# Performance work log

Measured on AMD Instinct MI355X. Metric: run time of the kernel, lower is better.

The kernel has to match this reference:

```python
import jax, jax.numpy as jnp
import numpy as np

TANH_CLIP = 10.0
TEMP = 1.0


def setup_inputs() -> dict:
    key = jax.random.key(0)
    ks = jax.random.split(key, 8)
    B, N, E, H, SC = 1024, 1000, 128, 8, 256
    dk = E // H
    context = jax.random.normal(ks[0], (B, 1, E), dtype=jnp.float32)
    step_context = jax.random.normal(ks[1], (B, 1, SC), dtype=jnp.float32)
    # scale weights so tanh/softmax stay in a sane numeric range
    W_step = jax.random.normal(ks[2], (E, SC), dtype=jnp.float32) * 0.05
    glimpse_K = jax.random.normal(ks[3], (H, B, 1, N, dk), dtype=jnp.float32)
    glimpse_V = jax.random.normal(ks[4], (H, B, 1, N, dk), dtype=jnp.float32)
    logit_K = jax.random.normal(ks[5], (B, 1, N, E), dtype=jnp.float32)
    W_out = jax.random.normal(ks[6], (E, E), dtype=jnp.float32) * 0.05
    mask = jax.random.randint(ks[7], (B, 1, N), 0, 2).astype(bool)
    mask = mask.at[:, :, 0].set(False)  # guarantee at least one feasible node
    return {"context": context, "step_context": step_context, "W_step": W_step,
            "glimpse_K": glimpse_K, "glimpse_V": glimpse_V, "logit_K": logit_K,
            "W_out": W_out, "mask": mask}


def reference(context, step_context, W_step, glimpse_K, glimpse_V, logit_K, W_out, mask):
    B, S, E = context.shape          # S = num_steps = 1
    H = glimpse_K.shape[0]
    dk = E // H
    neg_inf = jnp.float32(-jnp.inf)
    # query = context_node_projected + project_step_context(step_context)
    query = context + jnp.einsum('bsc,ec->bse', step_context, W_step)  # [B,S,E]
    # split heads: glimpse_Q -> [H,B,S,dk] (the singleton q-dim of the torch code is folded)
    Q = query.reshape(B, S, H, dk).transpose(2, 0, 1, 3)
    # compatibility [H,B,S,N]
    compat = jnp.einsum('hbsk,hbsnk->hbsn', Q, glimpse_K) / jnp.sqrt(jnp.float32(dk))
    compat = jnp.where(mask[None], neg_inf, compat)       # mask_inner
    attn = jax.nn.softmax(compat, axis=-1)
    heads = jnp.einsum('hbsn,hbsnk->hbsk', attn, glimpse_V)  # [H,B,S,dk]
    glimpse = heads.transpose(1, 2, 0, 3).reshape(B, S, E)   # concat heads
    glimpse = jnp.einsum('bse,oe->bso', glimpse, W_out)      # project_out
    # logits against logit_K  [B,S,N]
    logits = jnp.einsum('bse,bsne->bsn', glimpse, logit_K) / jnp.sqrt(jnp.float32(E))
    logits = jnp.tanh(logits) * jnp.float32(TANH_CLIP)       # tanh clipping
    logits = jnp.where(mask, neg_inf, logits)                # mask_logits
    log_p = jax.nn.log_softmax(logits / jnp.float32(TEMP), axis=-1)
    return log_p
```

## Files before the change

### kernel.cpp

```cpp
#include <hip/hip_runtime.h>
#include <hip/hip_bf16.h>
#include <math.h>

#define NB  1024
#define NN  1000
#define NE  128
#define NH  8
#define NDK 16
#define NSC 256

typedef __attribute__((ext_vector_type(4))) float f32x4;

__device__ __forceinline__ f32x4 ld4(const float* p) {
    return *reinterpret_cast<const f32x4*>(p);
}

__global__ __launch_bounds__(128)
void query_kernel(const float* __restrict__ ctx, const float* __restrict__ stepc,
                  const float* __restrict__ Wstep, float* __restrict__ q_ws)
{
    const int b = blockIdx.x, t = threadIdx.x;
    __shared__ float sc[NSC];
    sc[t] = stepc[b * NSC + t];
    sc[t + 128] = stepc[b * NSC + t + 128];
    __syncthreads();
    float acc = ctx[b * NE + t];
    const float4* w4 = reinterpret_cast<const float4*>(Wstep + (size_t)t * NSC);
    #pragma unroll 8
    for (int c4 = 0; c4 < NSC / 4; ++c4) {
        float4 w = w4[c4];
        acc += sc[4*c4] * w.x + sc[4*c4+1] * w.y + sc[4*c4+2] * w.z + sc[4*c4+3] * w.w;
    }
    q_ws[b * NE + t] = acc;
}

__global__ __launch_bounds__(256)
void attn_kernel(const float* __restrict__ q_ws,
                 const float* __restrict__ gK, const float* __restrict__ gV,
                 const unsigned char* __restrict__ mask,
                 float* __restrict__ heads_ws)
{
    const int bid = blockIdx.x;
    const int h = bid & (NH - 1);
    const int b = bid >> 3;
    const int t = threadIdx.x;
    const int w = t >> 6, lane = t & 63;
    const int qq  = lane & 3;
    const int rsl = lane >> 2;

    __shared__ float wmax[4], wsum[4];
    __shared__ __align__(16) float wred[4][16];

    const unsigned int* mw = reinterpret_cast<const unsigned int*>(mask);
    const bool m_i32 = (__ballot(mw[lane] <= 1u) == ~0ull);
    const int* mask_i = reinterpret_cast<const int*>(mask);

    const f32x4 qv = ld4(q_ws + (size_t)b * NE + h * NDK + qq * 4);

    int msk[16];
    #pragma unroll
    for (int i = 0; i < 16; ++i) {
        const int n = w * 16 + i * 64 + rsl;
        const bool dead = (n >= NN);
        const int nn = dead ? 0 : n;
        int mk = m_i32 ? (mask_i[(size_t)b * NN + nn] != 0)
                       : (mask[(size_t)b * NN + nn] != 0);
        msk[i] = mk | (dead ? 1 : 0);
    }

    const float* Kb = gK + (size_t)(h * NB + b) * NN * NDK;
    float pp[16];
    #pragma unroll
    for (int i = 0; i < 16; ++i) {
        const int n = w * 16 + i * 64 + rsl;
        const int nn = msk[i] ? 0 : n;
        f32x4 kv = ld4(Kb + (size_t)nn * NDK + qq * 4);
        pp[i] = kv.x*qv.x + kv.y*qv.y + kv.z*qv.z + kv.w*qv.w;
    }
    float sc[16];
    #pragma unroll
    for (int i = 0; i < 16; ++i) {
        float p = pp[i];
        p += __shfl_xor(p, 1);
        p += __shfl_xor(p, 2);
        sc[i] = msk[i] ? -INFINITY : p * 0.25f;
    }

    float m = sc[0];
    #pragma unroll
    for (int i = 1; i < 16; ++i) m = fmaxf(m, sc[i]);
    #pragma unroll
    for (int off = 32; off > 0; off >>= 1) m = fmaxf(m, __shfl_xor(m, off));
    if (lane == 0) wmax[w] = m;
    __syncthreads();
    const float M = fmaxf(fmaxf(wmax[0], wmax[1]), fmaxf(wmax[2], wmax[3]));

    float e[16], ls = 0.f;
    #pragma unroll
    for (int i = 0; i < 16; ++i) { e[i] = expf(sc[i] - M); ls += e[i]; }
    #pragma unroll
    for (int off = 32; off > 0; off >>= 1) ls += __shfl_xor(ls, off);
    if (lane == 0) wsum[w] = ls;

    const float* Vb = gV + (size_t)(h * NB + b) * NN * NDK;
    f32x4 acc = {0.f, 0.f, 0.f, 0.f};
    #pragma unroll
    for (int i = 0; i < 16; ++i) {
        const int n = w * 16 + i * 64 + rsl;
        const float p = e[i];
        const int nn = (p == 0.f) ? 0 : n;
        f32x4 vv = ld4(Vb + (size_t)nn * NDK + qq * 4);
        acc.x += p * vv.x; acc.y += p * vv.y; acc.z += p * vv.z; acc.w += p * vv.w;
    }
    #pragma unroll
    for (int off = 4; off < 64; off <<= 1) {
        acc.x += __shfl_xor(acc.x, off);
        acc.y += __shfl_xor(acc.y, off);
        acc.z += __shfl_xor(acc.z, off);
        acc.w += __shfl_xor(acc.w, off);
    }
    if (lane < 4) *reinterpret_cast<f32x4*>(&wred[w][lane * 4]) = acc;
    __syncthreads();

    if (t < NDK) {
        const float S = (wsum[0] + wsum[1] + wsum[2] + wsum[3]) * 0.25f;
        const float r = wred[0][t] + wred[1][t] + wred[2][t] + wred[3][t];
        heads_ws[(size_t)b * NE + h * NDK + t] = r / S;
    }
}

__global__ __launch_bounds__(512)
void logits_kernel(const float* __restrict__ heads_ws, const float* __restrict__ Wout,
                   const float* __restrict__ lK, const unsigned char* __restrict__ mask,
                   __hip_bfloat16* __restrict__ out)
{
    const int b = blockIdx.x, t = threadIdx.x;
    const int w = t >> 6, lane = t & 63;
    __shared__ __align__(16) float g[NE];
    __shared__ __align__(16) float gout[NE];
    __shared__ float red[8];
    __shared__ float Mv, LSv;

    const unsigned int* mw = reinterpret_cast<const unsigned int*>(mask);
    const bool m_i32 = (__ballot(mw[lane] <= 1u) == ~0ull);
    const int* mask_i = reinterpret_cast<const int*>(mask);

    if (t < NE) g[t] = heads_ws[(size_t)b * NE + t];
    __syncthreads();

    if (t < NE) {
        float acc = 0.f;
        const float4* w4 = reinterpret_cast<const float4*>(Wout + (size_t)t * NE);
        const float4* g4 = reinterpret_cast<const float4*>(g);
        #pragma unroll 8
        for (int e4 = 0; e4 < NE / 4; ++e4) {
            float4 wv = w4[e4]; float4 gg = g4[e4];
            acc += wv.x*gg.x + wv.y*gg.y + wv.z*gg.z + wv.w*gg.w;
        }
        gout[t] = acc;
    }
    __syncthreads();

    const f32x4* go4 = reinterpret_cast<const f32x4*>(gout);
    float lv[2];
    #pragma unroll
    for (int i = 0; i < 2; ++i) {
        const int n = t + 512 * i;
        const bool live = (n < NN);
        const int nidx = live ? n : 0;
        int mkd = m_i32 ? (mask_i[(size_t)b * NN + nidx] != 0)
                        : (mask[(size_t)b * NN + nidx] != 0);
        mkd |= (live ? 0 : 1);
        const int nn = mkd ? 0 : n;
        const float* lp = lK + ((size_t)b * NN + nn) * NE;
        float acc = 0.f;
        #pragma unroll
        for (int c4 = 0; c4 < NE / 4; ++c4) {
            f32x4 x = ld4(lp + 4 * c4);
            f32x4 gv = go4[c4];
            acc += x.x*gv.x + x.y*gv.y + x.z*gv.z + x.w*gv.w;
        }
        float val = tanhf(acc * 0.08838834764831845f) * 10.0f;
        lv[i] = mkd ? -3.0e38f : val;
    }

    float m = fmaxf(lv[0], lv[1]);
    #pragma unroll
    for (int off = 32; off > 0; off >>= 1) m = fmaxf(m, __shfl_xor(m, off));
    if (lane == 0) red[w] = m;
    __syncthreads();
    if (t == 0) {
        float mm = red[0];
        #pragma unroll
        for (int i = 1; i < 8; ++i) mm = fmaxf(mm, red[i]);
        Mv = mm;
    }
    __syncthreads();
    const float M = Mv;
    float s = expf(lv[0] - M) + expf(lv[1] - M);
    #pragma unroll
    for (int off = 32; off > 0; off >>= 1) s += __shfl_xor(s, off);
    if (lane == 0) red[w] = s;
    __syncthreads();
    if (t == 0) {
        float ss = 0.f;
        #pragma unroll
        for (int i = 0; i < 8; ++i) ss += red[i];
        LSv = M + logf(ss);
    }
    __syncthreads();
    const float LS = LSv;
    #pragma unroll
    for (int i = 0; i < 2; ++i) {
        const int n = t + 512 * i;
        if (n < NN)
            out[(size_t)b * NN + n] = __float2bfloat16(lv[i] - LS);
    }
}

__global__ __launch_bounds__(256, 4)
void evrp_decoder_fused(const float* __restrict__ ctx, const float* __restrict__ stepc,
                        const float* __restrict__ Wstep, const float* __restrict__ gK,
                        const float* __restrict__ gV, const float* __restrict__ lK,
                        const float* __restrict__ Wout, const unsigned char* __restrict__ mask,
                        __hip_bfloat16* __restrict__ out)
{
    const int b = blockIdx.x;
    const int t = threadIdx.x;
    __shared__ __align__(16) float q[NE];
    __shared__ __align__(16) float sc_l[NH * NN];
    __shared__ __align__(16) float g[NE];
    __shared__ __align__(16) float gout[NE];
    __shared__ __align__(16) float red[256];
    __shared__ __align__(16) float ovl[1024];
    __shared__ float mh[NH];
    __shared__ float rinv[NH];
    __shared__ float Mv, Sv;
    __shared__ int mtype;

    if (t == 0) {
        const unsigned int* mi = reinterpret_cast<const unsigned int*>(mask);
        int ok = 1;
        for (int i = 0; i < 64; ++i) ok = ok && (mi[i] <= 1u);
        mtype = ok;
    }
    red[t] = stepc[b * NSC + t];
    __syncthreads();
    const int m_i32 = mtype;
    if (t < NE) {
        float acc = ctx[b * NE + t];
        const float4* w4 = reinterpret_cast<const float4*>(Wstep + t * NSC);
        #pragma unroll 8
        for (int c4 = 0; c4 < NSC / 4; ++c4) {
            float4 w = w4[c4];
            acc += red[c4*4+0]*w.x + red[c4*4+1]*w.y + red[c4*4+2]*w.z + red[c4*4+3]*w.w;
        }
        q[t] = acc;
    }
    __syncthreads();
    const int* mask_i = reinterpret_cast<const int*>(mask);
    for (int n = t; n < NN; n += 256) {
        bool mk = m_i32 ? (mask_i[b * NN + n] != 0) : (mask[b * NN + n] != 0);
        if (mk) {
            #pragma unroll
            for (int h = 0; h < NH; ++h) sc_l[h * NN + n] = -INFINITY;
        } else {
            #pragma unroll
            for (int h = 0; h < NH; ++h) {
                const float4* k4 = reinterpret_cast<const float4*>(gK + (((size_t)h*NB + b)*NN + n)*NDK);
                const float4* q4 = reinterpret_cast<const float4*>(q + h * NDK);
                float acc = 0.f;
                #pragma unroll
                for (int i = 0; i < 4; ++i) {
                    float4 kv = k4[i]; float4 qv = q4[i];
                    acc += kv.x*qv.x + kv.y*qv.y + kv.z*qv.z + kv.w*qv.w;
                }
                sc_l[h * NN + n] = acc * 0.25f;
            }
        }
    }
    __syncthreads();
    {
        const int h = t >> 5, i = t & 31;
        float m = -INFINITY;
        for (int n = i; n < NN; n += 32) m = fmaxf(m, sc_l[h * NN + n]);
        red[t] = m;
        __syncthreads();
        if (t < NH) {
            float mm = -INFINITY;
            for (int i2 = 0; i2 < 32; ++i2) mm = fmaxf(mm, red[t * 32 + i2]);
            mh[t] = mm;
        }
        __syncthreads();
        const float mhh = mh[h];
        float s = 0.f;
        for (int n = i; n < NN; n += 32) {
            float ev = expf(sc_l[h * NN + n] - mhh);
            sc_l[h * NN + n] = ev;
            s += ev;
        }
        red[t] = s;
        __syncthreads();
        if (t < NH) {
            float ss = 0.f;
            for (int i2 = 0; i2 < 32; ++i2) ss += red[t * 32 + i2];
            rinv[t] = 1.0f / ss;
        }
        __syncthreads();
    }
    {
        float4* hp4 = reinterpret_cast<float4*>(ovl);
        const int h = t >> 5, rem = t & 31, kq = rem >> 3, j = rem & 7;
        const float* vbase = gV + (((size_t)h * NB + b) * NN) * NDK + kq * 4;
        float4 acc = {0.f, 0.f, 0.f, 0.f};
        for (int n = j; n < NN; n += 8) {
            float p = sc_l[h * NN + n];
            if (p != 0.f) {
                float4 v = *reinterpret_cast<const float4*>(vbase + (size_t)n * NDK);
                acc.x += p*v.x; acc.y += p*v.y; acc.z += p*v.z; acc.w += p*v.w;
            }
        }
        hp4[(h * 4 + kq) * 8 + j] = acc;
    }
    __syncthreads();
    if (t < NE) {
        const int h = t >> 4, k = t & 15, kq = k >> 2, kc = k & 3;
        float s = 0.f;
        #pragma unroll
        for (int j = 0; j < 8; ++j) s += ovl[((h * 4 + kq) * 8 + j) * 4 + kc];
        g[t] = s * rinv[h];
    }
    __syncthreads();
    if (t < NE) {
        float acc = 0.f;
        const float4* w4 = reinterpret_cast<const float4*>(Wout + t * NE);
        const float4* g4 = reinterpret_cast<const float4*>(g);
        #pragma unroll 8
        for (int e4 = 0; e4 < NE / 4; ++e4) {
            float4 w = w4[e4]; float4 gg = g4[e4];
            acc += w.x*gg.x + w.y*gg.y + w.z*gg.z + w.w*gg.w;
        }
        gout[t] = acc;
    }
    __syncthreads();
    float* llds = ovl;
    for (int n = t; n < NN; n += 256) {
        bool mk = m_i32 ? (mask_i[b * NN + n] != 0) : (mask[b * NN + n] != 0);
        float val;
        if (mk) val = -INFINITY;
        else {
            const float4* lk4 = reinterpret_cast<const float4*>(lK + ((size_t)b * NN + n) * NE);
            const float4* go4 = reinterpret_cast<const float4*>(gout);
            float acc = 0.f;
            #pragma unroll 8
            for (int e4 = 0; e4 < NE / 4; ++e4) {
                float4 lvv = lk4[e4]; float4 gv = go4[e4];
                acc += lvv.x*gv.x + lvv.y*gv.y + lvv.z*gv.z + lvv.w*gv.w;
            }
            val = tanhf(acc * 0.08838834764831845f) * 10.0f;
        }
        llds[n] = val;
    }
    __syncthreads();
    {
        float m = -INFINITY;
        for (int n = t; n < NN; n += 256) m = fmaxf(m, llds[n]);
        red[t] = m;
        __syncthreads();
        for (int s2 = 128; s2 > 0; s2 >>= 1) {
            if (t < s2) red[t] = fmaxf(red[t], red[t + s2]);
            __syncthreads();
        }
        if (t == 0) Mv = red[0];
        __syncthreads();
        const float M = Mv;
        float s = 0.f;
        for (int n = t; n < NN; n += 256) s += expf(llds[n] - M);
        red[t] = s;
        __syncthreads();
        for (int s2 = 128; s2 > 0; s2 >>= 1) {
            if (t < s2) red[t] += red[t + s2];
            __syncthreads();
        }
        if (t == 0) Sv = logf(red[0]);
        __syncthreads();
        const float LS = M + Sv;
        for (int n = t; n < NN; n += 256) {
            float l = llds[n];
            float r = (l == -INFINITY) ? -3.0e38f : (l - LS);
            out[(size_t)b * NN + n] = __float2bfloat16(r);
        }
    }
}

extern "C" void kernel_launch(void* const* d_in, const int* in_sizes, int n_in,
                              void* d_out, int out_size, void* d_ws, size_t ws_size,
                              hipStream_t stream) {
    const float* ctx   = (const float*)d_in[0];
    const float* stepc = (const float*)d_in[1];
    const float* Wstep = (const float*)d_in[2];
    const float* gK    = (const float*)d_in[3];
    const float* gV    = (const float*)d_in[4];
    const float* lK    = (const float*)d_in[5];
    const float* Wout  = (const float*)d_in[6];
    const unsigned char* mask = (const unsigned char*)d_in[7];
    __hip_bfloat16* out = (__hip_bfloat16*)d_out;

    const size_t need = (size_t)NB * NE * 4 * 2;
    if (ws_size >= need) {
        float* q_ws     = (float*)d_ws;
        float* heads_ws = q_ws + (size_t)NB * NE;
        query_kernel <<<dim3(NB),      dim3(128), 0, stream>>>(ctx, stepc, Wstep, q_ws);
        attn_kernel  <<<dim3(NB * NH), dim3(256), 0, stream>>>(q_ws, gK, gV, mask, heads_ws);
        logits_kernel<<<dim3(NB),      dim3(512), 0, stream>>>(heads_ws, Wout, lK, mask, out);
    } else {
        evrp_decoder_fused<<<dim3(NB), dim3(256), 0, stream>>>(
            ctx, stepc, Wstep, gK, gV, lK, Wout, mask, out);
    }
}
```

Measured before the change: 248.9 us.

## Issue K and V loads together and widen attention blocks to 512 threads

The attention kernel now uses 8 wavefronts per (batch, head) block, each thread covering 8 nodes instead of 16. The V rows are fetched in the same loop as the K rows, using the mask rather than the softmax result to skip masked rows. The exponentials are then fused directly into the V accumulation. The aim is to put more global loads in flight before the softmax barrier and so hide memory latency. In exchange, each thread keeps 8 V vectors in registers, and the cross-wavefront reductions become wider.

```diff
diff --git a/kernel.cpp b/kernel.cpp
--- a/kernel.cpp
+++ b/kernel.cpp
@@ -34,7 +34,7 @@
     q_ws[b * NE + t] = acc;
 }
 
-__global__ __launch_bounds__(256)
+__global__ __launch_bounds__(512, 6)
 void attn_kernel(const float* __restrict__ q_ws,
                  const float* __restrict__ gK, const float* __restrict__ gV,
                  const unsigned char* __restrict__ mask,
@@ -48,8 +48,8 @@
     const int qq  = lane & 3;
     const int rsl = lane >> 2;
 
-    __shared__ float wmax[4], wsum[4];
-    __shared__ __align__(16) float wred[4][16];
+    __shared__ float wmax[8], wsum[8];
+    __shared__ __align__(16) float wred[8][16];
 
     const unsigned int* mw = reinterpret_cast<const unsigned int*>(mask);
     const bool m_i32 = (__ballot(mw[lane] <= 1u) == ~0ull);
@@ -57,61 +57,62 @@
 
     const f32x4 qv = ld4(q_ws + (size_t)b * NE + h * NDK + qq * 4);
 
-    int msk[16];
-    #pragma unroll
-    for (int i = 0; i < 16; ++i) {
-        const int n = w * 16 + i * 64 + rsl;
+    unsigned mbits = 0;
+    #pragma unroll
+    for (int i = 0; i < 8; ++i) {
+        const int n = w * 16 + i * 128 + rsl;
         const bool dead = (n >= NN);
         const int nn = dead ? 0 : n;
         int mk = m_i32 ? (mask_i[(size_t)b * NN + nn] != 0)
                        : (mask[(size_t)b * NN + nn] != 0);
-        msk[i] = mk | (dead ? 1 : 0);
+        mbits |= (unsigned)(mk | (dead ? 1 : 0)) << i;
     }
 
     const float* Kb = gK + (size_t)(h * NB + b) * NN * NDK;
-    float pp[16];
-    #pragma unroll
-    for (int i = 0; i < 16; ++i) {
-        const int n = w * 16 + i * 64 + rsl;
-        const int nn = msk[i] ? 0 : n;
-        f32x4 kv = ld4(Kb + (size_t)nn * NDK + qq * 4);
-        pp[i] = kv.x*qv.x + kv.y*qv.y + kv.z*qv.z + kv.w*qv.w;
-    }
-    float sc[16];
-    #pragma unroll
-    for (int i = 0; i < 16; ++i) {
-        float p = pp[i];
+    const float* Vb = gV + (size_t)(h * NB + b) * NN * NDK;
+    f32x4 vreg[8];
+    float sc[8];
+    #pragma unroll
+    for (int i = 0; i < 8; ++i) {
+        const int n = w * 16 + i * 128 + rsl;
+        const int nn = ((mbits >> i) & 1u) ? 0 : n;
+        const size_t off = (size_t)nn * NDK + qq * 4;
+        f32x4 kv = ld4(Kb + off);
+        vreg[i] = ld4(Vb + off);
+        sc[i] = kv.x*qv.x + kv.y*qv.y + kv.z*qv.z + kv.w*qv.w;
+    }
+    #pragma unroll
+    for (int i = 0; i < 8; ++i) {
+        float p = sc[i];
         p += __shfl_xor(p, 1);
         p += __shfl_xor(p, 2);
-        sc[i] = msk[i] ? -INFINITY : p * 0.25f;
+        sc[i] = ((mbits >> i) & 1u) ? -INFINITY : p * 0.25f;
     }
 
     float m = sc[0];
     #pragma unroll
-    for (int i = 1; i < 16; ++i) m = fmaxf(m, sc[i]);
+    for (int i = 1; i < 8; ++i) m = fmaxf(m, sc[i]);
     #pragma unroll
     for (int off = 32; off > 0; off >>= 1) m = fmaxf(m, __shfl_xor(m, off));
     if (lane == 0) wmax[w] = m;
     __syncthreads();
-    const float M = fmaxf(fmaxf(wmax[0], wmax[1]), fmaxf(wmax[2], wmax[3]));
-
-    float e[16], ls = 0.f;
-    #pragma unroll
-    for (int i = 0; i < 16; ++i) { e[i] = expf(sc[i] - M); ls += e[i]; }
+    float M = wmax[0];
+    #pragma unroll
+    for (int i = 1; i < 8; ++i) M = fmaxf(M, wmax[i]);
+
+    f32x4 acc = {0.f, 0.f, 0.f, 0.f};
+    float ls = 0.f;
+    #pragma unroll
+    for (int i = 0; i < 8; ++i) {
+        const float e = expf(sc[i] - M);
+        ls += e;
+        acc.x += e * vreg[i].x; acc.y += e * vreg[i].y;
+        acc.z += e * vreg[i].z; acc.w += e * vreg[i].w;
+    }
     #pragma unroll
     for (int off = 32; off > 0; off >>= 1) ls += __shfl_xor(ls, off);
     if (lane == 0) wsum[w] = ls;
 
-    const float* Vb = gV + (size_t)(h * NB + b) * NN * NDK;
-    f32x4 acc = {0.f, 0.f, 0.f, 0.f};
-    #pragma unroll
-    for (int i = 0; i < 16; ++i) {
-        const int n = w * 16 + i * 64 + rsl;
-        const float p = e[i];
-        const int nn = (p == 0.f) ? 0 : n;
-        f32x4 vv = ld4(Vb + (size_t)nn * NDK + qq * 4);
-        acc.x += p * vv.x; acc.y += p * vv.y; acc.z += p * vv.z; acc.w += p * vv.w;
-    }
     #pragma unroll
     for (int off = 4; off < 64; off <<= 1) {
         acc.x += __shfl_xor(acc.x, off);
@@ -123,8 +124,13 @@
     __syncthreads();
 
     if (t < NDK) {
-        const float S = (wsum[0] + wsum[1] + wsum[2] + wsum[3]) * 0.25f;
-        const float r = wred[0][t] + wred[1][t] + wred[2][t] + wred[3][t];
+        float S = wsum[0];
+        #pragma unroll
+        for (int i = 1; i < 8; ++i) S += wsum[i];
+        S *= 0.25f;
+        float r = wred[0][t];
+        #pragma unroll
+        for (int i = 1; i < 8; ++i) r += wred[i][t];
         heads_ws[(size_t)b * NE + h * NDK + t] = r / S;
     }
 }
@@ -411,7 +417,7 @@
         float* q_ws     = (float*)d_ws;
         float* heads_ws = q_ws + (size_t)NB * NE;
         query_kernel <<<dim3(NB),      dim3(128), 0, stream>>>(ctx, stepc, Wstep, q_ws);
-        attn_kernel  <<<dim3(NB * NH), dim3(256), 0, stream>>>(q_ws, gK, gV, mask, heads_ws);
+        attn_kernel  <<<dim3(NB * NH), dim3(512), 0, stream>>>(q_ws, gK, gV, mask, heads_ws);
         logits_kernel<<<dim3(NB),      dim3(512), 0, stream>>>(heads_ws, Wout, lK, mask, out);
     } else {
         evrp_decoder_fused<<<dim3(NB), dim3(256), 0, stream>>>(
```

Result: faster. 232.4 us (-6.6%).
